# Kernel tuning notes

Hardware: AMD Instinct MI355X
Metric: run time of the kernel (lower is better)

Reference implementation:

```python
import jax, jax.numpy as jnp
import numpy as np

N, E, F, T, C, HOR = 50000, 800000, 4, 12, 32, 12


def setup_inputs() -> dict:
    key = jax.random.key(0)
    ks = jax.random.split(key, 24)
    def rn(k, shape, s=0.1):
        return jax.random.normal(k, shape, jnp.float32) * s
    inp = {
        "x": jax.random.normal(ks[0], (N, F, T), jnp.float32),
        "edge_index": jax.random.randint(ks[1], (2, E), 0, N, dtype=jnp.int64),
        "edge_weight": jax.random.uniform(ks[2], (E,), jnp.float32),
        "attention": jax.random.uniform(ks[3], (T,), jnp.float32),
    }
    names = ["Wz", "bz", "Wlz", "blz", "Wr", "br", "Wlr", "blr", "Wh", "bh", "Wlh", "blh"]
    shapes = [(F, C), (C,), (2 * C, C), (C,), (F, C), (C,), (2 * C, C), (C,), (F, C), (C,), (2 * C, C), (C,)]
    for i, (n, s) in enumerate(zip(names, shapes)):
        inp[n] = rn(ks[4 + i], s)
    inp["Wout"] = rn(ks[20], (C, HOR))
    inp["bout"] = jnp.zeros((HOR,), jnp.float32)
    return inp


def reference(x, edge_index, edge_weight, attention,
              Wz, bz, Wlz, blz, Wr, br, Wlr, blr, Wh, bh, Wlh, blh,
              Wout, bout):
    n = x.shape[0]
    c = Wz.shape[1]
    row, col = edge_index[0], edge_index[1]

    # GCN normalization with self-loops (weight 1): A_hat = D^-1/2 (A+I) D^-1/2
    deg = jax.ops.segment_sum(edge_weight, col, num_segments=n) + 1.0
    dis = 1.0 / jnp.sqrt(deg)                      # deg >= 1 thanks to self-loop
    norm = dis[row] * edge_weight * dis[col]       # [E]
    self_norm = dis * dis                          # [N] self-loop coefficient

    def conv(xt, W, b):
        # xt: [N, F] -> [N, C]; sparse normalized aggregation over edge list
        xw = xt @ W
        agg = jax.ops.segment_sum(norm[:, None] * xw[row], col, num_segments=n)
        return agg + self_norm[:, None] * xw + b

    probs = jax.nn.softmax(attention)              # attention over periods
    H0 = jnp.zeros((n, c), x.dtype)                # A3TGCN passes H=None each period
    H_accum = jnp.zeros((n, c), x.dtype)
    for t in range(x.shape[2]):                    # fixed small period loop (as original)
        xt = x[:, :, t]
        Z = jax.nn.sigmoid(jnp.concatenate([conv(xt, Wz, bz), H0], axis=1) @ Wlz + blz)
        R = jax.nn.sigmoid(jnp.concatenate([conv(xt, Wr, br), H0], axis=1) @ Wlr + blr)
        Ht = jnp.tanh(jnp.concatenate([conv(xt, Wh, bh), H0 * R], axis=1) @ Wlh + blh)
        Hn = Z * H0 + (1.0 - Z) * Ht               # GRU update from zero state
        H_accum = H_accum + probs[t] * Hn

    h = jax.nn.relu(H_accum)
    return h @ Wout + bout
```

## Files before the change

### kernel.cpp

```cpp
#include <hip/hip_runtime.h>
#include <hip/hip_bf16.h>

#define NN 50000
#define NE 800000
#define FD 4
#define TD 12
#define CD 32
#define HD 12
#define FT 48
#define NBANK 8

#define OFF_HEAD   0
#define OFF_PAY    400000
#define OFF_DIS    3600000
#define OFF_CST    3650000

__global__ void build_pre_kernel(const int* __restrict__ ei, const float* __restrict__ w,
                                 int* __restrict__ head, int4* __restrict__ pay4,
                                 const float* __restrict__ Wz, const float* __restrict__ bz,
                                 const float* __restrict__ Wlz, const float* __restrict__ blz,
                                 const float* __restrict__ Wh, const float* __restrict__ bh,
                                 const float* __restrict__ Wlh, const float* __restrict__ blh,
                                 const float* __restrict__ attention,
                                 float* __restrict__ cst) {
    int tid = threadIdx.x;
    if (blockIdx.x < (NE / 256)) {
        int e = blockIdx.x * 256 + tid;
        int r = ei[e];
        int c = ei[NE + e];
        int old = atomicExch(&head[(e & (NBANK-1)) * NN + c], e);
        pay4[e] = make_int4(r, __float_as_int(w[e]), old, 0);
        return;
    }
    if (tid < 128) {
        int f = tid >> 5, c = tid & 31;
        float s = 0.f, s2 = 0.f;
        #pragma unroll
        for (int k = 0; k < 32; ++k) {
            s  += Wz[f*32 + k] * Wlz[k*32 + c];
            s2 += Wh[f*32 + k] * Wlh[k*32 + c];
        }
        cst[tid]       = s;
        cst[160 + tid] = s2;
    } else if (tid < 160) {
        int c = tid - 128;
        float s = blz[c], s2 = blh[c];
        #pragma unroll
        for (int k = 0; k < 32; ++k) {
            s  += bz[k] * Wlz[k*32 + c];
            s2 += bh[k] * Wlh[k*32 + c];
        }
        cst[128 + c] = s;
        cst[288 + c] = s2;
    } else if (tid == 160) {
        float m = -1e30f;
        for (int t = 0; t < TD; ++t) m = fmaxf(m, attention[t]);
        float e[TD], s = 0.f;
        #pragma unroll
        for (int t = 0; t < TD; ++t) { e[t] = __expf(attention[t] - m); s += e[t]; }
        float inv = 1.f / s;
        #pragma unroll
        for (int t = 0; t < TD; ++t) cst[320 + t] = e[t] * inv;
    }
}

__global__ void degdis_kernel(const int* __restrict__ head, const int4* __restrict__ pay4,
                              float* __restrict__ dis) {
    int t = blockIdx.x * blockDim.x + threadIdx.x;
    int i = t >> 3;
    int b = t & 7;
    if (i >= NN) return;
    float s = 0.f;
    int e = head[b * NN + i];
    while (e >= 0) {
        int4 p = pay4[e];
        s += __int_as_float(p.y);
        e = p.z;
    }
    s += __shfl_xor(s, 1, 8);
    s += __shfl_xor(s, 2, 8);
    s += __shfl_xor(s, 4, 8);
    if (b == 0) dis[i] = rsqrtf(s + 1.0f);
}

__global__ __launch_bounds__(256) void gather_gru_kernel(
        const float* __restrict__ x, const float* __restrict__ dis,
        const int* __restrict__ head, const int4* __restrict__ pay4,
        const float* __restrict__ cst, const float* __restrict__ Wout,
        const float* __restrict__ bout, float* __restrict__ out) {
    __shared__ int2  smeta[16][64];
    __shared__ float sy[16][FT];
    __shared__ float hbuf[16][CD];
    __shared__ float sAz[128], sAh[128], sCz[32], sCh[32], sP[TD];
    __shared__ float sWout[CD * HD], sBout[HD];

    int tid = threadIdx.x;
    if (tid < 128) { sAz[tid] = cst[tid]; sAh[tid] = cst[160 + tid]; }
    if (tid < 32)  { sCz[tid] = cst[128 + tid]; sCh[tid] = cst[288 + tid]; }
    if (tid < TD)  { sP[tid] = cst[320 + tid]; sBout[tid] = bout[tid]; }
    for (int k = tid; k < CD * HD; k += 256) sWout[k] = Wout[k];
    __syncthreads();

    int g  = tid & 15;
    int ln = tid >> 4;
    int i  = blockIdx.x * 16 + ln;

    const float3* x3 = (const float3*)x;
    float d = dis[i];
    float3 a = x3[i * 16 + g];
    float ax = 0.f, ay = 0.f, az = 0.f;

    int e = (g < 8) ? head[g * NN + i] : -1;

    while (true) {
        int r0=0,r1=0,r2=0,r3=0,r4=0,r5=0,r6=0,r7=0;
        float n0=0,n1=0,n2=0,n3=0,n4=0,n5=0,n6=0,n7=0;
        int cnt = 0;
        #define STEP(RK,NK) if (e >= 0) { int4 p = pay4[e]; RK = p.x; \
            NK = dis[p.x] * __int_as_float(p.y); e = p.z; ++cnt; }
        STEP(r0,n0) STEP(r1,n1) STEP(r2,n2) STEP(r3,n3)
        STEP(r4,n4) STEP(r5,n5) STEP(r6,n6) STEP(r7,n7)
        #undef STEP

        int incl = cnt;
        #pragma unroll
        for (int dd = 1; dd < 8; dd <<= 1) {
            int t2 = __shfl_up(incl, dd, 16);
            if (g >= dd) incl += t2;
        }
        int S = __shfl(incl, 7, 16);
        if (S == 0) break;
        int off = incl - cnt;

        if (cnt > 0) smeta[ln][off + 0] = make_int2(r0, __float_as_int(n0));
        if (cnt > 1) smeta[ln][off + 1] = make_int2(r1, __float_as_int(n1));
        if (cnt > 2) smeta[ln][off + 2] = make_int2(r2, __float_as_int(n2));
        if (cnt > 3) smeta[ln][off + 3] = make_int2(r3, __float_as_int(n3));
        if (cnt > 4) smeta[ln][off + 4] = make_int2(r4, __float_as_int(n4));
        if (cnt > 5) smeta[ln][off + 5] = make_int2(r5, __float_as_int(n5));
        if (cnt > 6) smeta[ln][off + 6] = make_int2(r6, __float_as_int(n6));
        if (cnt > 7) smeta[ln][off + 7] = make_int2(r7, __float_as_int(n7));
        __builtin_amdgcn_wave_barrier();

        #pragma unroll 8
        for (int k = 0; k < S; ++k) {
            int2 m = smeta[ln][k];
            float nv = __int_as_float(m.y);
            float3 v = x3[m.x * 16 + g];
            ax += nv * v.x; ay += nv * v.y; az += nv * v.z;
        }
    }

    {
        float s0 = d * d;
        sy[ln][g*3 + 0] = a.x * s0 + d * ax;
        sy[ln][g*3 + 1] = a.y * s0 + d * ay;
        sy[ln][g*3 + 2] = a.z * s0 + d * az;
    }
    __syncthreads();

    {
        int c0 = g, c1 = g + 16;
        float az00 = sAz[c0], az01 = sAz[32+c0], az02 = sAz[64+c0], az03 = sAz[96+c0];
        float az10 = sAz[c1], az11 = sAz[32+c1], az12 = sAz[64+c1], az13 = sAz[96+c1];
        float ah00 = sAh[c0], ah01 = sAh[32+c0], ah02 = sAh[64+c0], ah03 = sAh[96+c0];
        float ah10 = sAh[c1], ah11 = sAh[32+c1], ah12 = sAh[64+c1], ah13 = sAh[96+c1];
        float cz0 = sCz[c0], cz1 = sCz[c1], ch0 = sCh[c0], ch1 = sCh[c1];

        float hacc0 = 0.f, hacc1 = 0.f;
        #pragma unroll
        for (int t = 0; t < TD; ++t) {
            float y0 = sy[ln][0*TD + t];
            float y1 = sy[ln][1*TD + t];
            float y2 = sy[ln][2*TD + t];
            float y3 = sy[ln][3*TD + t];
            float z0 = cz0 + y0*az00 + y1*az01 + y2*az02 + y3*az03;
            float z1 = cz1 + y0*az10 + y1*az11 + y2*az12 + y3*az13;
            float h0 = ch0 + y0*ah00 + y1*ah01 + y2*ah02 + y3*ah03;
            float h1 = ch1 + y0*ah10 + y1*ah11 + y2*ah12 + y3*ah13;
            float Z0 = 1.f / (1.f + __expf(-z0));
            float Z1 = 1.f / (1.f + __expf(-z1));
            float e0 = __expf(2.f * h0);
            float e1 = __expf(2.f * h1);
            float H0v = (e0 - 1.f) / (e0 + 1.f);
            float H1v = (e1 - 1.f) / (e1 + 1.f);
            float p = sP[t];
            hacc0 += p * (1.f - Z0) * H0v;
            hacc1 += p * (1.f - Z1) * H1v;
        }
        hbuf[ln][c0] = fmaxf(hacc0, 0.f);
        hbuf[ln][c1] = fmaxf(hacc1, 0.f);
    }
    __syncthreads();

    if (tid < 16 * HD) {
        int lnode = tid / HD, hor = tid - lnode * HD;
        int gn = blockIdx.x * 16 + lnode;
        float s = sBout[hor];
        #pragma unroll
        for (int k = 0; k < CD; ++k) s += hbuf[lnode][k] * sWout[k * HD + hor];
        out[gn * HD + hor] = s;
    }
}

extern "C" void kernel_launch(void* const* d_in, const int* in_sizes, int n_in,
                              void* d_out, int out_size, void* d_ws, size_t ws_size,
                              hipStream_t stream) {
    const float* x      = (const float*)d_in[0];
    const int*   ei     = (const int*)d_in[1];
    const float* ew     = (const float*)d_in[2];
    const float* attn   = (const float*)d_in[3];
    const float* Wz     = (const float*)d_in[4];
    const float* bz     = (const float*)d_in[5];
    const float* Wlz    = (const float*)d_in[6];
    const float* blz    = (const float*)d_in[7];
    const float* Wh     = (const float*)d_in[12];
    const float* bh     = (const float*)d_in[13];
    const float* Wlh    = (const float*)d_in[14];
    const float* blh    = (const float*)d_in[15];
    const float* Wout   = (const float*)d_in[16];
    const float* bout   = (const float*)d_in[17];
    float* out = (float*)d_out;

    float* ws   = (float*)d_ws;
    int*   head = (int*)(ws + OFF_HEAD);
    int4*  pay4 = (int4*)(ws + OFF_PAY);
    float* dis  = ws + OFF_DIS;
    float* cst  = ws + OFF_CST;

    hipMemsetAsync(head, 0xFF, NBANK * NN * sizeof(int), stream);

    build_pre_kernel<<<NE / 256 + 1, 256, 0, stream>>>(ei, ew, head, pay4,
                                                       Wz, bz, Wlz, blz,
                                                       Wh, bh, Wlh, blh, attn, cst);

    degdis_kernel<<<(NN * 8 + 255) / 256, 256, 0, stream>>>(head, pay4, dis);

    gather_gru_kernel<<<NN / 16, 256, 0, stream>>>(
        x, dis, head, pay4, cst, Wout, bout, out);
}
```

Before: 198.2 us.

## Accumulate banked degrees atomically and pre-scale features by inverse sqrt degree

Degree sums are now accumulated with banked float atomics during edge list construction, so the separate linked-list walk for degrees is no longer needed. A new kernel reduces the eight banks, computes dis, and writes a pre-scaled copy xs = dis*x. The gather loop then no longer performs the dependent dis[row] lookup per edge, and the self-loop term folds into the accumulator. The cost is an extra memset, extra atomics, and a full write and reread of x.

```diff
diff --git a/kernel.cpp b/kernel.cpp
--- a/kernel.cpp
+++ b/kernel.cpp
@@ -11,12 +11,15 @@
 #define NBANK 8
 
 #define OFF_HEAD   0
-#define OFF_PAY    400000
-#define OFF_DIS    3600000
-#define OFF_CST    3650000
+#define OFF_DEG8   400000
+#define OFF_PAY    800000
+#define OFF_DIS    4000000
+#define OFF_XS     4050000
+#define OFF_CST    6450000
 
 __global__ void build_pre_kernel(const int* __restrict__ ei, const float* __restrict__ w,
-                                 int* __restrict__ head, int4* __restrict__ pay4,
+                                 int* __restrict__ head, float* __restrict__ deg8,
+                                 int4* __restrict__ pay4,
                                  const float* __restrict__ Wz, const float* __restrict__ bz,
                                  const float* __restrict__ Wlz, const float* __restrict__ blz,
                                  const float* __restrict__ Wh, const float* __restrict__ bh,
@@ -28,8 +31,11 @@
         int e = blockIdx.x * 256 + tid;
         int r = ei[e];
         int c = ei[NE + e];
-        int old = atomicExch(&head[(e & (NBANK-1)) * NN + c], e);
-        pay4[e] = make_int4(r, __float_as_int(w[e]), old, 0);
+        float we = w[e];
+        int bank = (e & (NBANK-1)) * NN + c;
+        int old = atomicExch(&head[bank], e);
+        atomicAdd(&deg8[bank], we);
+        pay4[e] = make_int4(r, __float_as_int(we), old, 0);
         return;
     }
     if (tid < 128) {
@@ -64,27 +70,25 @@
     }
 }
 
-__global__ void degdis_kernel(const int* __restrict__ head, const int4* __restrict__ pay4,
-                              float* __restrict__ dis) {
+__global__ void disxs_kernel(const float* __restrict__ deg8, const float* __restrict__ x,
+                             float* __restrict__ dis, float* __restrict__ xs) {
     int t = blockIdx.x * blockDim.x + threadIdx.x;
-    int i = t >> 3;
-    int b = t & 7;
-    if (i >= NN) return;
-    float s = 0.f;
-    int e = head[b * NN + i];
-    while (e >= 0) {
-        int4 p = pay4[e];
-        s += __int_as_float(p.y);
-        e = p.z;
-    }
-    s += __shfl_xor(s, 1, 8);
-    s += __shfl_xor(s, 2, 8);
-    s += __shfl_xor(s, 4, 8);
-    if (b == 0) dis[i] = rsqrtf(s + 1.0f);
+    int i = t >> 4;
+    int g = t & 15;
+    float v = (g < 8) ? deg8[g * NN + i] : 0.f;
+    v += __shfl_xor(v, 1, 8);
+    v += __shfl_xor(v, 2, 8);
+    v += __shfl_xor(v, 4, 8);
+    float dsum = __shfl(v, 0, 16);
+    float di = rsqrtf(dsum + 1.0f);
+    if (g == 0) dis[i] = di;
+    const float3* x3 = (const float3*)x;
+    float3 xv = x3[i * 16 + g];
+    ((float3*)xs)[i * 16 + g] = make_float3(di * xv.x, di * xv.y, di * xv.z);
 }
 
 __global__ __launch_bounds__(256) void gather_gru_kernel(
-        const float* __restrict__ x, const float* __restrict__ dis,
+        const float* __restrict__ xs, const float* __restrict__ dis,
         const int* __restrict__ head, const int4* __restrict__ pay4,
         const float* __restrict__ cst, const float* __restrict__ Wout,
         const float* __restrict__ bout, float* __restrict__ out) {
@@ -105,10 +109,10 @@
     int ln = tid >> 4;
     int i  = blockIdx.x * 16 + ln;
 
-    const float3* x3 = (const float3*)x;
+    const float3* xs3 = (const float3*)xs;
     float d = dis[i];
-    float3 a = x3[i * 16 + g];
-    float ax = 0.f, ay = 0.f, az = 0.f;
+    float3 a = xs3[i * 16 + g];
+    float ax = a.x, ay = a.y, az = a.z;
 
     int e = (g < 8) ? head[g * NN + i] : -1;
 
@@ -117,7 +121,7 @@
         float n0=0,n1=0,n2=0,n3=0,n4=0,n5=0,n6=0,n7=0;
         int cnt = 0;
         #define STEP(RK,NK) if (e >= 0) { int4 p = pay4[e]; RK = p.x; \
-            NK = dis[p.x] * __int_as_float(p.y); e = p.z; ++cnt; }
+            NK = __int_as_float(p.y); e = p.z; ++cnt; }
         STEP(r0,n0) STEP(r1,n1) STEP(r2,n2) STEP(r3,n3)
         STEP(r4,n4) STEP(r5,n5) STEP(r6,n6) STEP(r7,n7)
         #undef STEP
@@ -146,17 +150,14 @@
         for (int k = 0; k < S; ++k) {
             int2 m = smeta[ln][k];
             float nv = __int_as_float(m.y);
-            float3 v = x3[m.x * 16 + g];
+            float3 v = xs3[m.x * 16 + g];
             ax += nv * v.x; ay += nv * v.y; az += nv * v.z;
         }
     }
 
-    {
-        float s0 = d * d;
-        sy[ln][g*3 + 0] = a.x * s0 + d * ax;
-        sy[ln][g*3 + 1] = a.y * s0 + d * ay;
-        sy[ln][g*3 + 2] = a.z * s0 + d * az;
-    }
+    sy[ln][g*3 + 0] = d * ax;
+    sy[ln][g*3 + 1] = d * ay;
+    sy[ln][g*3 + 2] = d * az;
     __syncthreads();
 
     {
@@ -224,18 +225,21 @@
 
     float* ws   = (float*)d_ws;
     int*   head = (int*)(ws + OFF_HEAD);
+    float* deg8 = ws + OFF_DEG8;
     int4*  pay4 = (int4*)(ws + OFF_PAY);
     float* dis  = ws + OFF_DIS;
+    float* xs   = ws + OFF_XS;
     float* cst  = ws + OFF_CST;
 
     hipMemsetAsync(head, 0xFF, NBANK * NN * sizeof(int), stream);
-
-    build_pre_kernel<<<NE / 256 + 1, 256, 0, stream>>>(ei, ew, head, pay4,
+    hipMemsetAsync(deg8, 0x00, NBANK * NN * sizeof(float), stream);
+
+    build_pre_kernel<<<NE / 256 + 1, 256, 0, stream>>>(ei, ew, head, deg8, pay4,
                                                        Wz, bz, Wlz, blz,
                                                        Wh, bh, Wlh, blh, attn, cst);
 
-    degdis_kernel<<<(NN * 8 + 255) / 256, 256, 0, stream>>>(head, pay4, dis);
+    disxs_kernel<<<NN * 16 / 256, 256, 0, stream>>>(deg8, x, dis, xs);
 
     gather_gru_kernel<<<NN / 16, 256, 0, stream>>>(
-        x, dis, head, pay4, cst, Wout, bout, out);
-}
+        xs, dis, head, pay4, cst, Wout, bout, out);
+}
```

New measurement: 239.9 us. 21.0% more time.
